# Kernel tuning notes

Measured on AMD Instinct MI355X. Metric: run time of the kernel, lower is better.

Reference implementation:

```python
import jax, jax.numpy as jnp
import numpy as np

N = 20000       # num_nodes
E = 200000      # ~ N*N*0.0005 directed edges from erdos_renyi
IN = 64         # in_channels
HID = 128       # hidden_channels (per head)
H = 4           # heads
OUT = 10        # out_channels
K1 = 10000      # ceil(0.5*N) nodes kept by pool1 (single graph -> static)
K2 = 5000       # ceil(0.5*K1) kept by pool2
NEG_SLOPE = 0.2 # PyG GATConv default negative_slope


def setup_inputs() -> dict:
    key = jax.random.key(0)
    ks = jax.random.split(key, 16)
    def glorot(k, shp, fan):
        return (jax.random.normal(k, shp, jnp.float32) / np.sqrt(fan)).astype(jnp.float32)
    x = jax.random.normal(ks[0], (N, IN), jnp.float32)
    edge_index = jax.random.randint(ks[1], (2, E), 0, N, dtype=jnp.int32)
    batch = jnp.zeros((N,), jnp.int32)
    W1 = glorot(ks[2], (IN, H * HID), IN)
    a_src1 = glorot(ks[3], (H, HID), HID)
    a_dst1 = glorot(ks[4], (H, HID), HID)
    b1 = jnp.zeros((H * HID,), jnp.float32)
    pw1 = glorot(ks[5], (H * HID,), H * HID)
    W2 = glorot(ks[6], (H * HID, H * HID), H * HID)
    a_src2 = glorot(ks[7], (H, HID), HID)
    a_dst2 = glorot(ks[8], (H, HID), HID)
    b2 = jnp.zeros((H * HID,), jnp.float32)
    pw2 = glorot(ks[9], (H * HID,), H * HID)
    Wl = glorot(ks[10], (H * HID, OUT), H * HID)
    bl = jnp.zeros((OUT,), jnp.float32)
    return dict(x=x, edge_index=edge_index, batch=batch,
                W1=W1, a_src1=a_src1, a_dst1=a_dst1, b1=b1, pw1=pw1,
                W2=W2, a_src2=a_src2, a_dst2=a_dst2, b2=b2, pw2=pw2,
                Wl=Wl, bl=bl)


def _gat(x, src, dst, emask, W, a_src, a_dst, bias):
    """PyG GATConv: gather -> LeakyReLU edge score -> scatter-softmax over dst -> scatter-add.
    Self-loops added (PyG default). emask marks valid edges (invalid edges point at node 0)."""
    n = x.shape[0]
    Hh, C = a_src.shape
    h = (x @ W).reshape(n, Hh, C)                      # [n,H,C]
    asrc = jnp.einsum('nhc,hc->nh', h, a_src)          # [n,H]
    adst = jnp.einsum('nhc,hc->nh', h, a_dst)
    loops = jnp.arange(n, dtype=src.dtype)
    sa = jnp.concatenate([src, loops])                 # [E+n]
    da = jnp.concatenate([dst, loops])
    ma = jnp.concatenate([emask, jnp.ones((n,), bool)])
    logit = jax.nn.leaky_relu(asrc[sa] + adst[da], negative_slope=NEG_SLOPE)  # [E+n,H]
    logit = jnp.where(ma[:, None], logit, -1e9)
    mx = jax.ops.segment_max(logit, da, num_segments=n)        # every node has a self-loop
    e = jnp.where(ma[:, None], jnp.exp(logit - mx[da]), 0.0)
    den = jax.ops.segment_sum(e, da, num_segments=n)
    alpha = e / den[da]                                         # [E+n,H]
    msg = (alpha[:, :, None] * h[sa]).reshape(-1, Hh * C)       # [E+n,H*C]
    return jax.ops.segment_sum(msg, da, num_segments=n) + bias  # concat heads + bias


def _topk_pool(x, src, dst, emask, w, k):
    """PyG TopKPooling (single graph): score = tanh(x.w/||w||), keep top-k nodes,
    scale kept features by score, relabel & mask edges between kept nodes."""
    score = jnp.tanh((x @ w) / jnp.linalg.norm(w))     # [n]
    vals, perm = jax.lax.top_k(score, k)
    xn = x[perm] * vals[:, None]                       # [k,F]
    remap = jnp.full((x.shape[0],), -1, jnp.int32).at[perm].set(jnp.arange(k, dtype=jnp.int32))
    s2 = remap[src]
    d2 = remap[dst]
    m2 = emask & (s2 >= 0) & (d2 >= 0)
    return xn, jnp.where(m2, s2, 0), jnp.where(m2, d2, 0), m2


def reference(x, edge_index, batch, W1, a_src1, a_dst1, b1, pw1,
              W2, a_src2, a_dst2, b2, pw2, Wl, bl):
    src = edge_index[0]
    dst = edge_index[1]
    mask = jnp.ones((src.shape[0],), bool)
    h = jax.nn.elu(_gat(x, src, dst, mask, W1, a_src1, a_dst1, b1))
    h, src, dst, mask = _topk_pool(h, src, dst, mask, pw1, K1)
    h = jax.nn.elu(_gat(h, src, dst, mask, W2, a_src2, a_dst2, b2))
    h, src, dst, mask = _topk_pool(h, src, dst, mask, pw2, K2)
    g = jnp.mean(h, axis=0, keepdims=True)             # global_mean_pool, single graph
    return g @ Wl + bl                                  # [1, OUT]
```

## Files before the change

### kernel.cpp

```cpp
#include <hip/hip_runtime.h>
#include <math.h>

#define N_NODES 20000
#define E_EDGES 200000
#define K1_KEEP 10000
#define K2_KEEP 5000
#define HIDC 128
#define NHEAD 4
#define FDIM 512
#define NEG 0.2f
#define BSTRIDE 64
#define SELCAP 20
#define MPAD 10112
#define FR_GRID 250
#define FR_RPB 40

typedef _Float16 half8 __attribute__((ext_vector_type(8)));
typedef _Float16 half4 __attribute__((ext_vector_type(4)));
typedef float f32x4 __attribute__((ext_vector_type(4)));

__device__ __forceinline__ float leaky(float x){ return x > 0.f ? x : NEG * x; }
__device__ __forceinline__ float elu(float x){ return x > 0.f ? x : expm1f(x); }
__device__ __forceinline__ unsigned ordkey(float f){
    unsigned u = __float_as_uint(f);
    return (u & 0x80000000u) ? ~u : (u | 0x80000000u);
}

template<int K, int COLB, int AMODE, bool GATHER, bool CLEAR>
__global__ __launch_bounds__(256) void gemm_tile(const float* __restrict__ A,
        const float* __restrict__ W, _Float16* __restrict__ out,
        const int* __restrict__ gidx, const float* __restrict__ gsc,
        const float* __restrict__ avS, const float* __restrict__ avD,
        float* __restrict__ asrc, float* __restrict__ adst, int n,
        int ngemm, int* __restrict__ ctmp, int cn,
        const float* __restrict__ cw, float* __restrict__ cinvn)
{
    int t = threadIdx.x;
    int bid = blockIdx.x;
    if constexpr (CLEAR){
        if (bid >= ngemm){
            __shared__ float redc[4];
            int b2 = bid - ngemm;
            int i = b2 * 256 + t;
            if (i < cn) ctmp[i] = 0;
            if (b2 == 0){
                float s = cw[t] * cw[t] + cw[t + 256] * cw[t + 256];
#pragma unroll
                for (int off = 32; off > 0; off >>= 1) s += __shfl_xor(s, off);
                if ((t & 63) == 0) redc[t >> 6] = s;
                __syncthreads();
                if (t == 0) *cinvn = rsqrtf(redc[0] + redc[1] + redc[2] + redc[3]);
            }
            return;
        }
    }
    constexpr int NR = COLB / 16;
    constexpr int WPT = COLB / 32;
    constexpr int BPR = 512 / COLB;
    __shared__ float At[32][68];
    __shared__ float Wt[32][COLB];
    int row0 = (bid / BPR) * 64;
    int col0 = (bid % BPR) * COLB;
    int tr = t >> 4;
    int tc = t & 15;
    float acc[4][NR] = {};

    int arow[2]; float asc[2];
#pragma unroll
    for (int i = 0; i < 2; ++i){
        int r = (t + i * 256) >> 3;
        int gr = row0 + r;
        arow[i] = -1; asc[i] = 1.f;
        if (gr < n){
            if (GATHER){ arow[i] = gidx[gr]; asc[i] = gsc[arow[i]]; }
            else arow[i] = gr;
        }
    }

    float4 pa[2], pw[WPT];
#pragma unroll
    for (int i = 0; i < 2; ++i){
        int kq = (t + i * 256) & 7;
        pa[i] = make_float4(0.f, 0.f, 0.f, 0.f);
        if (arow[i] >= 0){
            pa[i] = *reinterpret_cast<const float4*>(&A[(size_t)arow[i] * K + kq * 4]);
            if (GATHER){ pa[i].x *= asc[i]; pa[i].y *= asc[i]; pa[i].z *= asc[i]; pa[i].w *= asc[i]; }
        }
    }
#pragma unroll
    for (int i = 0; i < WPT; ++i){
        int s = t + i * 256; int k = s / (COLB / 4), c4 = s % (COLB / 4);
        pw[i] = *reinterpret_cast<const float4*>(&W[(size_t)k * 512 + col0 + c4 * 4]);
    }

    for (int kc = 0; kc < K; kc += 32){
#pragma unroll
        for (int i = 0; i < 2; ++i){
            int s = t + i * 256; int r = s >> 3, kq = s & 7;
            At[kq * 4 + 0][r] = pa[i].x;
            At[kq * 4 + 1][r] = pa[i].y;
            At[kq * 4 + 2][r] = pa[i].z;
            At[kq * 4 + 3][r] = pa[i].w;
        }
#pragma unroll
        for (int i = 0; i < WPT; ++i){
            int s = t + i * 256; int k = s / (COLB / 4), c4 = s % (COLB / 4);
            *reinterpret_cast<float4*>(&Wt[k][c4 * 4]) = pw[i];
        }
        __syncthreads();
        if (kc + 32 < K){
            int kn = kc + 32;
#pragma unroll
            for (int i = 0; i < 2; ++i){
                int kq = (t + i * 256) & 7;
                pa[i] = make_float4(0.f, 0.f, 0.f, 0.f);
                if (arow[i] >= 0){
                    pa[i] = *reinterpret_cast<const float4*>(&A[(size_t)arow[i] * K + kn + kq * 4]);
                    if (GATHER){ pa[i].x *= asc[i]; pa[i].y *= asc[i]; pa[i].z *= asc[i]; pa[i].w *= asc[i]; }
                }
            }
#pragma unroll
            for (int i = 0; i < WPT; ++i){
                int s = t + i * 256; int k = s / (COLB / 4), c4 = s % (COLB / 4);
                pw[i] = *reinterpret_cast<const float4*>(&W[(size_t)(kn + k) * 512 + col0 + c4 * 4]);
            }
        }
#pragma unroll 8
        for (int kk = 0; kk < 32; ++kk){
            float4 a = *reinterpret_cast<const float4*>(&At[kk][tr * 4]);
            float af[4] = {a.x, a.y, a.z, a.w};
            float wf[NR];
            {
                float4 w0 = *reinterpret_cast<const float4*>(&Wt[kk][tc * 4]);
                wf[0] = w0.x; wf[1] = w0.y; wf[2] = w0.z; wf[3] = w0.w;
                if constexpr (NR == 8){
                    float4 w1 = *reinterpret_cast<const float4*>(&Wt[kk][tc * 4 + 64]);
                    wf[4] = w1.x; wf[5] = w1.y; wf[6] = w1.z; wf[7] = w1.w;
                }
            }
#pragma unroll
            for (int r = 0; r < 4; ++r)
#pragma unroll
                for (int c = 0; c < NR; ++c) acc[r][c] += af[r] * wf[c];
        }
        __syncthreads();
    }
#pragma unroll
    for (int r = 0; r < 4; ++r){
        int gr = row0 + 4 * tr + r;
        if (gr < n){
            half4 h0, h1q;
#pragma unroll
            for (int c = 0; c < 4; ++c) h0[c] = (_Float16)acc[r][c];
            *reinterpret_cast<half4*>(&out[(size_t)gr * 512 + col0 + tc * 4]) = h0;
            if constexpr (NR == 8){
#pragma unroll
                for (int c = 0; c < 4; ++c) h1q[c] = (_Float16)acc[r][4 + c];
                *reinterpret_cast<half4*>(&out[(size_t)gr * 512 + col0 + 64 + tc * 4]) = h1q;
            }
        }
    }
    if constexpr (AMODE == 1){
        int head = col0 >> 7;
        const float* as = avS + head * HIDC;
        const float* ad = avD + head * HIDC;
#pragma unroll
        for (int r = 0; r < 4; ++r){
            float s = 0.f, d = 0.f;
#pragma unroll
            for (int c = 0; c < 4; ++c){
                s += acc[r][c] * as[4 * tc + c];
                d += acc[r][c] * ad[4 * tc + c];
                s += acc[r][4 + c] * as[64 + 4 * tc + c];
                d += acc[r][4 + c] * ad[64 + 4 * tc + c];
            }
#pragma unroll
            for (int off = 1; off < 16; off <<= 1){ s += __shfl_xor(s, off); d += __shfl_xor(d, off); }
            int gr = row0 + 4 * tr + r;
            if (tc == 0 && gr < n){ asrc[gr * 4 + head] = s; adst[gr * 4 + head] = d; }
        }
    }
}

__global__ __launch_bounds__(256) void prep_w2(const float* __restrict__ W2,
        _Float16* __restrict__ B0, _Float16* __restrict__ B1)
{
    __shared__ float tile[32][33];
    int bn = blockIdx.x & 15, bk = blockIdx.x >> 4;
    int n0 = bn * 32, k0 = bk * 32;
    int t = threadIdx.x;
    int j = t & 31, i0 = t >> 5;
#pragma unroll
    for (int ii = 0; ii < 32; ii += 8)
        tile[i0 + ii][j] = W2[(size_t)(k0 + i0 + ii) * 512 + n0 + j];
    __syncthreads();
#pragma unroll
    for (int ii = 0; ii < 32; ii += 8){
        float v = tile[j][i0 + ii];
        _Float16 h0 = (_Float16)v;
        _Float16 h1 = (_Float16)(v - (float)h0);
        size_t o = (size_t)(n0 + i0 + ii) * 512 + k0 + j;
        B0[o] = h0; B1[o] = h1;
    }
}

__global__ __launch_bounds__(256) void prep_a(const float* __restrict__ out1,
        const int* __restrict__ oldi, const float* __restrict__ score,
        _Float16* __restrict__ A0, _Float16* __restrict__ A1)
{
    int tid = blockIdx.x * 256 + threadIdx.x;
    int r = tid >> 6, kq = (tid & 63) << 3;
    half8 v0 = (half8)0, v1 = (half8)0;
    if (r < K1_KEEP){
        int o = oldi[r];
        float sc = score[o];
        const float4* p = reinterpret_cast<const float4*>(&out1[(size_t)o * 512 + kq]);
        float4 x0 = p[0], x1 = p[1];
        float vals[8] = {x0.x, x0.y, x0.z, x0.w, x1.x, x1.y, x1.z, x1.w};
#pragma unroll
        for (int j = 0; j < 8; ++j){
            float v = vals[j] * sc;
            _Float16 h = (_Float16)v;
            v0[j] = h;
            v1[j] = (_Float16)(v - (float)h);
        }
    }
    *reinterpret_cast<half8*>(&A0[(size_t)r * 512 + kq]) = v0;
    *reinterpret_cast<half8*>(&A1[(size_t)r * 512 + kq]) = v1;
}

__global__ __launch_bounds__(256, 2) void gemm2_mfma(
        const _Float16* __restrict__ A0, const _Float16* __restrict__ A1,
        const _Float16* __restrict__ B0, const _Float16* __restrict__ B1,
        const float* __restrict__ avS, const float* __restrict__ avD,
        _Float16* __restrict__ C, float* __restrict__ asrc, float* __restrict__ adst)
{
    __shared__ _Float16 smem[2][4][128][32];
    int t = threadIdx.x;
    int l = t & 63, w = t >> 6;
    int wr = w >> 1, wc = w & 1;
    int bidn = blockIdx.x & 3, bidm = blockIdx.x >> 2;
    int row0 = bidm * 128, col0 = bidn * 128;

    const _Float16* plane = (w == 0) ? A0 : (w == 1) ? A1 : (w == 2) ? B0 : B1;
    int prow0 = (w < 2) ? row0 : col0;
    int mloc = l >> 2;
    int gsw = (l & 3) ^ (mloc & 3);
    const _Float16* gbase = plane + (size_t)(prow0 + mloc) * 512 + gsw * 8;

    f32x4 acc[4][4];
#pragma unroll
    for (int m = 0; m < 4; ++m)
#pragma unroll
        for (int n = 0; n < 4; ++n) acc[m][n] = (f32x4){0.f, 0.f, 0.f, 0.f};

    auto stage = [&](int buf, int chunk){
        const _Float16* src = gbase + chunk * 32;
        char* db = (char*)&smem[buf][w][0][0];
#pragma unroll
        for (int i = 0; i < 8; ++i)
            __builtin_amdgcn_global_load_lds(
                (const __attribute__((address_space(1))) void*)(src + (size_t)i * 8192),
                (__attribute__((address_space(3))) void*)(db + i * 1024), 16, 0, 0);
    };

    int rb = (l & 15) * 64 + (((l >> 4) ^ (l & 3)) * 16);
    const char* sb = (const char*)smem;

    stage(0, 0);
    __syncthreads();
    for (int c = 0; c < 16; ++c){
        int buf = c & 1;
        if (c < 15) stage(buf ^ 1, c + 1);
        const char* base = sb + buf * 32768;
        half8 a0[4], a1[4], b0[4], b1[4];
#pragma unroll
        for (int m = 0; m < 4; ++m){
            a0[m] = *(const half8*)(base +         wr * 4096 + m * 1024 + rb);
            a1[m] = *(const half8*)(base +  8192 + wr * 4096 + m * 1024 + rb);
            b0[m] = *(const half8*)(base + 16384 + wc * 4096 + m * 1024 + rb);
            b1[m] = *(const half8*)(base + 24576 + wc * 4096 + m * 1024 + rb);
        }
#pragma unroll
        for (int m = 0; m < 4; ++m)
#pragma unroll
            for (int n = 0; n < 4; ++n)
                acc[m][n] = __builtin_amdgcn_mfma_f32_16x16x32_f16(a0[m], b0[n], acc[m][n], 0, 0, 0);
#pragma unroll
        for (int m = 0; m < 4; ++m)
#pragma unroll
            for (int n = 0; n < 4; ++n)
                acc[m][n] = __builtin_amdgcn_mfma_f32_16x16x32_f16(a0[m], b1[n], acc[m][n], 0, 0, 0);
#pragma unroll
        for (int m = 0; m < 4; ++m)
#pragma unroll
            for (int n = 0; n < 4; ++n)
                acc[m][n] = __builtin_amdgcn_mfma_f32_16x16x32_f16(a1[m], b0[n], acc[m][n], 0, 0, 0);
        __syncthreads();
    }

    int head = bidn;
    const float* asv = avS + head * HIDC + wc * 64;
    const float* adv = avD + head * HIDC + wc * 64;
    int lc = l & 15, lg = l >> 4;
    int rbase = row0 + wr * 64;
    int cbase = col0 + wc * 64;
#pragma unroll
    for (int m = 0; m < 4; ++m){
#pragma unroll
        for (int q = 0; q < 4; ++q){
            int row = rbase + m * 16 + lg * 4 + q;
            bool ok = row < K1_KEEP;
            float s = 0.f, d = 0.f;
#pragma unroll
            for (int n = 0; n < 4; ++n){
                float v = acc[m][n][q];
                int cc = n * 16 + lc;
                if (ok) C[(size_t)row * 512 + cbase + cc] = (_Float16)v;
                s += v * asv[cc];
                d += v * adv[cc];
            }
#pragma unroll
            for (int off = 1; off < 16; off <<= 1){
                s += __shfl_xor(s, off);
                d += __shfl_xor(d, off);
            }
            if (ok && lc == 0){
                asrc[row * 8 + head * 2 + wc] = s;
                adst[row * 8 + head * 2 + wc] = d;
            }
        }
    }
}

__global__ void edge_fill(const int* __restrict__ src, const int* __restrict__ dst, int e,
                          int* __restrict__ tmp, int* __restrict__ csr){
    int i = blockIdx.x * 256 + threadIdx.x;
    if (i >= e) return;
    int d = dst[i];
    int pos = atomicAdd(&tmp[d], 1);
    if (pos < BSTRIDE) csr[d * BSTRIDE + pos] = src[i];
}

template<bool FILTER>
__global__ __launch_bounds__(256) void gat_fused(const _Float16* __restrict__ h,
        const float* __restrict__ asrc, const float* __restrict__ adst,
        const int* __restrict__ degs, const int* __restrict__ csr,
        const int* __restrict__ oldi, const int* __restrict__ remap,
        const float* __restrict__ bias, const float* __restrict__ pw,
        const float* __restrict__ invn, float* __restrict__ out,
        float* __restrict__ score, int n)
{
    int node = blockIdx.x * 4 + (threadIdx.x >> 6);
    int lane = threadIdx.x & 63;
    if (node >= n) return;
    int od = FILTER ? oldi[node] : node;
    int deg = degs[od]; if (deg > BSTRIDE) deg = BSTRIDE;
    int e0 = od * BSTRIDE;
    int ph = lane & 3;
    int pe = lane >> 2;
    float adn, sown;
    if (FILTER){
        float2 dv = *reinterpret_cast<const float2*>(&adst[(size_t)node * 8 + ph * 2]);
        float2 sv = *reinterpret_cast<const float2*>(&asrc[(size_t)node * 8 + ph * 2]);
        adn = dv.x + dv.y; sown = sv.x + sv.y;
    } else {
        adn = adst[node * 4 + ph]; sown = asrc[node * 4 + ph];
    }
    float slog = leaky(sown + adn);
    int sreg[4];
    float mx = slog;
#pragma unroll
    for (int blk = 0; blk < 4; ++blk){
        int j = blk * 16 + pe;
        int s = -1;
        if (j < deg){
            s = csr[e0 + j];
            if (FILTER) s = remap[s];
            if (s >= 0){
                float av;
                if (FILTER){
                    float2 v = *reinterpret_cast<const float2*>(&asrc[(size_t)s * 8 + ph * 2]);
                    av = v.x + v.y;
                } else av = asrc[s * 4 + ph];
                mx = fmaxf(mx, leaky(av + adn));
            }
        }
        sreg[blk] = s;
    }
#pragma unroll
    for (int off = 4; off < 64; off <<= 1) mx = fmaxf(mx, __shfl_xor(mx, off));
    float aexp[4];
    float lsum = 0.f;
#pragma unroll
    for (int blk = 0; blk < 4; ++blk){
        float ex = 0.f;
        int s = sreg[blk];
        if (s >= 0){
            float av;
            if (FILTER){
                float2 v = *reinterpret_cast<const float2*>(&asrc[(size_t)s * 8 + ph * 2]);
                av = v.x + v.y;
            } else av = asrc[s * 4 + ph];
            ex = expf(leaky(av + adn) - mx);
        }
        aexp[blk] = ex;
        lsum += ex;
    }
#pragma unroll
    for (int off = 4; off < 64; off <<= 1) lsum += __shfl_xor(lsum, off);
    float es  = expf(slog - mx);
    float inv = 1.f / (lsum + es);

    int f0 = lane * 8;
    int hf = lane >> 4;
    float invh  = __shfl(inv, hf);
    float aself = __shfl(es, hf) * invh;
    float4 acc0, acc1;
    {
        half8 v = *reinterpret_cast<const half8*>(&h[(size_t)node * FDIM + f0]);
        acc0 = make_float4(aself * (float)v[0], aself * (float)v[1],
                           aself * (float)v[2], aself * (float)v[3]);
        acc1 = make_float4(aself * (float)v[4], aself * (float)v[5],
                           aself * (float)v[6], aself * (float)v[7]);
    }
#pragma unroll
    for (int blk = 0; blk < 4; ++blk){
        int base = blk * 16;
        if (base >= deg) break;
        int cnt = deg - base; if (cnt > 16) cnt = 16;
        for (int e = 0; e < cnt; ++e){
            int s = __shfl(sreg[blk], e * 4);
            if (FILTER && s < 0) continue;
            float al = __shfl(aexp[blk], e * 4 + hf) * invh;
            half8 u = *reinterpret_cast<const half8*>(&h[(size_t)s * FDIM + f0]);
            acc0.x += al * (float)u[0]; acc0.y += al * (float)u[1];
            acc0.z += al * (float)u[2]; acc0.w += al * (float)u[3];
            acc1.x += al * (float)u[4]; acc1.y += al * (float)u[5];
            acc1.z += al * (float)u[6]; acc1.w += al * (float)u[7];
        }
    }
    const float4* bp = reinterpret_cast<const float4*>(&bias[f0]);
    float4 b0 = bp[0], b1 = bp[1];
    float4 o0 = make_float4(elu(acc0.x + b0.x), elu(acc0.y + b0.y),
                            elu(acc0.z + b0.z), elu(acc0.w + b0.w));
    float4 o1 = make_float4(elu(acc1.x + b1.x), elu(acc1.y + b1.y),
                            elu(acc1.z + b1.z), elu(acc1.w + b1.w));
    float4* op = reinterpret_cast<float4*>(&out[(size_t)node * FDIM + f0]);
    op[0] = o0; op[1] = o1;
    const float4* wp = reinterpret_cast<const float4*>(&pw[f0]);
    float4 w0 = wp[0], w1 = wp[1];
    float s = o0.x * w0.x + o0.y * w0.y + o0.z * w0.z + o0.w * w0.w
            + o1.x * w1.x + o1.y * w1.y + o1.z * w1.z + o1.w * w1.w;
#pragma unroll
    for (int off = 32; off > 0; off >>= 1) s += __shfl_xor(s, off);
    if (lane == 0) score[node] = tanhf(s * (*invn));
}

__global__ __launch_bounds__(1024) void select_compact(const float* __restrict__ score,
        int n, int k, int* __restrict__ remap, int* __restrict__ oldidx,
        float* __restrict__ zbuf, int zn,
        const float* __restrict__ w, float* __restrict__ invn)
{
    __shared__ unsigned hist[16][256];
    __shared__ unsigned wtot[4];
    __shared__ unsigned s_prefix, s_rem, l_tie, l_keep;
    __shared__ float red2[16];
    int t = threadIdx.x;
    int wv = t >> 6;
    unsigned keys[SELCAP];
#pragma unroll
    for (int j = 0; j < SELCAP; ++j){
        int i = t + j * 1024;
        keys[j] = (i < n) ? ordkey(score[i]) : 0u;
    }
    if (t == 0){ s_prefix = 0u; s_rem = (unsigned)k; l_tie = 0u; l_keep = 0u; }
    for (int i = t; i < 16 * 256; i += 1024) ((unsigned*)hist)[i] = 0u;
    if (zbuf && t < zn) zbuf[t] = 0.f;
    __syncthreads();
    for (int pass = 3; pass >= 0; --pass){
        unsigned shift = (unsigned)pass * 8u;
        unsigned pmask = (pass == 3) ? 0u : (0xFFFFFFFFu << (shift + 8u));
        unsigned pref = s_prefix;
        unsigned remv = s_rem;
#pragma unroll
        for (int j = 0; j < SELCAP; ++j){
            int i = t + j * 1024;
            if (i < n && (keys[j] & pmask) == pref)
                atomicAdd(&hist[wv][(keys[j] >> shift) & 255u], 1u);
        }
        __syncthreads();
        unsigned c = 0, v = 0;
        if (t < 256){
            unsigned a = 0;
#pragma unroll
            for (int wq = 0; wq < 16; ++wq) a += hist[wq][t];
            c = a; v = a;
#pragma unroll
            for (int off = 1; off < 64; off <<= 1){
                unsigned o = __shfl_down(v, off);
                if ((t & 63) + off < 64) v += o;
            }
            if ((t & 63) == 0) wtot[t >> 6] = v;
        }
        __syncthreads();
        if (t < 256){
#pragma unroll
            for (int q = 0; q < 4; ++q)
                if (q > (t >> 6)) v += wtot[q];
            unsigned nxt = v - c;
            if (v >= remv && nxt < remv){
                s_prefix = pref | ((unsigned)t << shift);
                s_rem = remv - nxt;
            }
        }
        __syncthreads();
        if (pass > 0){
            for (int i = t; i < 16 * 256; i += 1024) ((unsigned*)hist)[i] = 0u;
            __syncthreads();
        }
    }
    unsigned T = s_prefix, ties = s_rem;
#pragma unroll
    for (int j = 0; j < SELCAP; ++j){
        int i = t + j * 1024;
        if (i >= n) continue;
        unsigned key = keys[j];
        int keep = 0;
        if (key > T) keep = 1;
        else if (key == T){
            unsigned tk = atomicAdd(&l_tie, 1u);
            if (tk < ties) keep = 1;
        }
        if (keep){
            int pos = (int)atomicAdd(&l_keep, 1u);
            remap[i] = pos;
            oldidx[pos] = i;
        } else remap[i] = -1;
    }
    if (w){
        float s = (t < 512) ? w[t] * w[t] : 0.f;
#pragma unroll
        for (int off = 32; off > 0; off >>= 1) s += __shfl_xor(s, off);
        if ((t & 63) == 0) red2[wv] = s;
        __syncthreads();
        if (t == 0){
            float a = 0.f;
            for (int i = 0; i < 16; ++i) a += red2[i];
            *invn = rsqrtf(a);
        }
    }
}

__global__ __launch_bounds__(512) void final_reduce(const float* __restrict__ x,
        const int* __restrict__ remap, const float* __restrict__ score,
        float* __restrict__ acc, const float* __restrict__ Wl)
{
    __shared__ float gsh[512];
    int t = threadIdx.x;
    int r0 = blockIdx.x * FR_RPB;
    float a = 0.f;
#pragma unroll
    for (int i = 0; i < FR_RPB; i += 4){
        int rr = r0 + i;
        float s0 = (remap[rr + 0] >= 0) ? score[rr + 0] : 0.f;
        float s1 = (remap[rr + 1] >= 0) ? score[rr + 1] : 0.f;
        float s2 = (remap[rr + 2] >= 0) ? score[rr + 2] : 0.f;
        float s3 = (remap[rr + 3] >= 0) ? score[rr + 3] : 0.f;
        float v0 = x[(size_t)(rr + 0) * FDIM + t];
        float v1 = x[(size_t)(rr + 1) * FDIM + t];
        float v2 = x[(size_t)(rr + 2) * FDIM + t];
        float v3 = x[(size_t)(rr + 3) * FDIM + t];
        a += v0 * s0 + v1 * s1 + v2 * s2 + v3 * s3;
    }
    gsh[t] = a;
    __syncthreads();
    int wv = t >> 6, lane = t & 63;
#pragma unroll
    for (int rep = 0; rep < 2; ++rep){
        int w = wv + rep * 8;
        if (w >= 10) break;
        float s = 0.f;
#pragma unroll
        for (int f = 0; f < 8; ++f) s += gsh[lane + f * 64] * Wl[(lane + f * 64) * 10 + w];
#pragma unroll
        for (int off = 32; off > 0; off >>= 1) s += __shfl_xor(s, off);
        if (lane == 0) atomicAdd(&acc[w * 32], s);
    }
}

__global__ __launch_bounds__(64) void final_out(const float* __restrict__ acc,
        const float* __restrict__ bl, float* __restrict__ out)
{
    int t = threadIdx.x;
    if (t < 10) out[t] = acc[t * 32] * (1.0f / K2_KEEP) + bl[t];
}

extern "C" void kernel_launch(void* const* d_in, const int* in_sizes, int n_in,
                              void* d_out, int out_size, void* d_ws, size_t ws_size,
                              hipStream_t stream)
{
    (void)in_sizes; (void)n_in; (void)out_size; (void)ws_size;
    const float* x   = (const float*)d_in[0];
    const int*   ei  = (const int*)  d_in[1];
    const float* W1  = (const float*)d_in[3];
    const float* as1 = (const float*)d_in[4];
    const float* ad1 = (const float*)d_in[5];
    const float* b1  = (const float*)d_in[6];
    const float* pw1 = (const float*)d_in[7];
    const float* W2  = (const float*)d_in[8];
    const float* as2 = (const float*)d_in[9];
    const float* ad2 = (const float*)d_in[10];
    const float* b2  = (const float*)d_in[11];
    const float* pw2 = (const float*)d_in[12];
    const float* Wl  = (const float*)d_in[13];
    const float* bl  = (const float*)d_in[14];
    const int* src1 = ei;
    const int* dst1 = ei + E_EDGES;

    char* wsb = (char*)d_ws;
    size_t off = 0;
    auto alloc = [&](size_t bytes) -> char* {
        char* p = wsb + off;
        off += (bytes + 255) & ~(size_t)255;
        return p;
    };
    _Float16* h1f = (_Float16*)alloc((size_t)N_NODES * FDIM * 2);
    float* out1 = (float*)alloc((size_t)N_NODES * FDIM * 4);
    float* asrc = (float*)alloc((size_t)N_NODES * NHEAD * 4);
    float* adst = (float*)alloc((size_t)N_NODES * NHEAD * 4);
    float* score= (float*)alloc((size_t)N_NODES * 4);
    float* invn = (float*)alloc(4);
    int* tmp  = (int*)alloc((size_t)N_NODES * 4);
    int* csr  = (int*)alloc((size_t)N_NODES * BSTRIDE * 4);
    int* remap= (int*)alloc((size_t)N_NODES * 4);
    int* oldi = (int*)alloc((size_t)K1_KEEP * 4);
    float* racc = (float*)alloc(320 * 4);
    _Float16* a0p = (_Float16*)alloc((size_t)MPAD * FDIM * 2);
    _Float16* a1p = (_Float16*)alloc((size_t)MPAD * FDIM * 2);
    _Float16* w2t0 = (_Float16*)alloc((size_t)FDIM * FDIM * 2);
    _Float16* w2t1 = (_Float16*)alloc((size_t)FDIM * FDIM * 2);
    _Float16* h2f = h1f;
    float* out2 = out1;

    int gx1 = (N_NODES + 63) / 64;
    int ngemm1 = gx1 * 4;
    int nclr = (N_NODES + 255) / 256;
    gemm_tile<64, 128, 1, false, true><<<ngemm1 + nclr, 256, 0, stream>>>(x, W1, h1f,
            nullptr, nullptr, as1, ad1, asrc, adst, N_NODES,
            ngemm1, tmp, N_NODES, pw1, invn);
    prep_w2<<<256, 256, 0, stream>>>(W2, w2t0, w2t1);
    edge_fill<<<(E_EDGES + 255) / 256, 256, 0, stream>>>(src1, dst1, E_EDGES, tmp, csr);
    gat_fused<false><<<(N_NODES + 3) / 4, 256, 0, stream>>>(h1f, asrc, adst, tmp, csr,
            nullptr, nullptr, b1, pw1, invn, out1, score, N_NODES);

    select_compact<<<1, 1024, 0, stream>>>(score, N_NODES, K1_KEEP, remap, oldi,
                                           nullptr, 0, pw2, invn);

    prep_a<<<MPAD / 4, 256, 0, stream>>>(out1, oldi, score, a0p, a1p);
    gemm2_mfma<<<(MPAD / 128) * 4, 256, 0, stream>>>(a0p, a1p, w2t0, w2t1,
            as2, ad2, h2f, asrc, adst);
    gat_fused<true><<<(K1_KEEP + 3) / 4, 256, 0, stream>>>(h2f, asrc, adst, tmp, csr,
            oldi, remap, b2, pw2, invn, out2, score, K1_KEEP);

    select_compact<<<1, 1024, 0, stream>>>(score, K1_KEEP, K2_KEEP, remap, oldi,
                                           racc, 320, nullptr, nullptr);
    final_reduce<<<FR_GRID, 512, 0, stream>>>(out2, remap, score, racc, Wl);
    final_out<<<1, 64, 0, stream>>>(racc, bl, (float*)d_out);
}
```

Measured before the change: 274.2 us.

## Move first GAT projection onto split-fp16 MFMA GEMM path

Replaces the fp32 SIMT tiled GEMM for x@W1 with the templated MFMA GEMM already used for layer two. Inputs and weights are split into hi/lo fp16 planes to keep accuracy close to fp32. The MFMA kernel writes attention logits in the 8-wide partial layout, so the unfiltered GAT path now reads that layout too. This adds two prep kernels (x split, W1 transpose/split merged with the counter clear and norm) and extra memory traffic in exchange for matrix-core throughput.

```diff
diff --git a/kernel.cpp b/kernel.cpp
--- a/kernel.cpp
+++ b/kernel.cpp
@@ -12,6 +12,7 @@
 #define BSTRIDE 64
 #define SELCAP 20
 #define MPAD 10112
+#define MPAD1 20096
 #define FR_GRID 250
 #define FR_RPB 40
 
@@ -26,159 +27,62 @@
     return (u & 0x80000000u) ? ~u : (u | 0x80000000u);
 }
 
-template<int K, int COLB, int AMODE, bool GATHER, bool CLEAR>
-__global__ __launch_bounds__(256) void gemm_tile(const float* __restrict__ A,
-        const float* __restrict__ W, _Float16* __restrict__ out,
-        const int* __restrict__ gidx, const float* __restrict__ gsc,
-        const float* __restrict__ avS, const float* __restrict__ avD,
-        float* __restrict__ asrc, float* __restrict__ adst, int n,
-        int ngemm, int* __restrict__ ctmp, int cn,
+__global__ __launch_bounds__(256) void prep_x(const float* __restrict__ x,
+        _Float16* __restrict__ X0, _Float16* __restrict__ X1)
+{
+    int tid = blockIdx.x * 256 + threadIdx.x;
+    int r = tid >> 3, c8 = (tid & 7) << 3;
+    half8 v0 = (half8)0, v1 = (half8)0;
+    if (r < N_NODES){
+        const float4* p = reinterpret_cast<const float4*>(&x[(size_t)r * 64 + c8]);
+        float4 x0 = p[0], x1 = p[1];
+        float vals[8] = {x0.x, x0.y, x0.z, x0.w, x1.x, x1.y, x1.z, x1.w};
+#pragma unroll
+        for (int j = 0; j < 8; ++j){
+            _Float16 h = (_Float16)vals[j];
+            v0[j] = h;
+            v1[j] = (_Float16)(vals[j] - (float)h);
+        }
+    }
+    *reinterpret_cast<half8*>(&X0[(size_t)r * 64 + c8]) = v0;
+    *reinterpret_cast<half8*>(&X1[(size_t)r * 64 + c8]) = v1;
+}
+
+__global__ __launch_bounds__(256) void prep_w1x(const float* __restrict__ W1,
+        _Float16* __restrict__ B0, _Float16* __restrict__ B1,
+        int* __restrict__ ctmp, int cn,
         const float* __restrict__ cw, float* __restrict__ cinvn)
 {
+    int bid = blockIdx.x;
     int t = threadIdx.x;
-    int bid = blockIdx.x;
-    if constexpr (CLEAR){
-        if (bid >= ngemm){
-            __shared__ float redc[4];
-            int b2 = bid - ngemm;
-            int i = b2 * 256 + t;
-            if (i < cn) ctmp[i] = 0;
-            if (b2 == 0){
-                float s = cw[t] * cw[t] + cw[t + 256] * cw[t + 256];
-#pragma unroll
-                for (int off = 32; off > 0; off >>= 1) s += __shfl_xor(s, off);
-                if ((t & 63) == 0) redc[t >> 6] = s;
-                __syncthreads();
-                if (t == 0) *cinvn = rsqrtf(redc[0] + redc[1] + redc[2] + redc[3]);
-            }
-            return;
-        }
-    }
-    constexpr int NR = COLB / 16;
-    constexpr int WPT = COLB / 32;
-    constexpr int BPR = 512 / COLB;
-    __shared__ float At[32][68];
-    __shared__ float Wt[32][COLB];
-    int row0 = (bid / BPR) * 64;
-    int col0 = (bid % BPR) * COLB;
-    int tr = t >> 4;
-    int tc = t & 15;
-    float acc[4][NR] = {};
-
-    int arow[2]; float asc[2];
-#pragma unroll
-    for (int i = 0; i < 2; ++i){
-        int r = (t + i * 256) >> 3;
-        int gr = row0 + r;
-        arow[i] = -1; asc[i] = 1.f;
-        if (gr < n){
-            if (GATHER){ arow[i] = gidx[gr]; asc[i] = gsc[arow[i]]; }
-            else arow[i] = gr;
-        }
-    }
-
-    float4 pa[2], pw[WPT];
-#pragma unroll
-    for (int i = 0; i < 2; ++i){
-        int kq = (t + i * 256) & 7;
-        pa[i] = make_float4(0.f, 0.f, 0.f, 0.f);
-        if (arow[i] >= 0){
-            pa[i] = *reinterpret_cast<const float4*>(&A[(size_t)arow[i] * K + kq * 4]);
-            if (GATHER){ pa[i].x *= asc[i]; pa[i].y *= asc[i]; pa[i].z *= asc[i]; pa[i].w *= asc[i]; }
-        }
-    }
-#pragma unroll
-    for (int i = 0; i < WPT; ++i){
-        int s = t + i * 256; int k = s / (COLB / 4), c4 = s % (COLB / 4);
-        pw[i] = *reinterpret_cast<const float4*>(&W[(size_t)k * 512 + col0 + c4 * 4]);
-    }
-
-    for (int kc = 0; kc < K; kc += 32){
-#pragma unroll
-        for (int i = 0; i < 2; ++i){
-            int s = t + i * 256; int r = s >> 3, kq = s & 7;
-            At[kq * 4 + 0][r] = pa[i].x;
-            At[kq * 4 + 1][r] = pa[i].y;
-            At[kq * 4 + 2][r] = pa[i].z;
-            At[kq * 4 + 3][r] = pa[i].w;
-        }
-#pragma unroll
-        for (int i = 0; i < WPT; ++i){
-            int s = t + i * 256; int k = s / (COLB / 4), c4 = s % (COLB / 4);
-            *reinterpret_cast<float4*>(&Wt[k][c4 * 4]) = pw[i];
-        }
-        __syncthreads();
-        if (kc + 32 < K){
-            int kn = kc + 32;
-#pragma unroll
-            for (int i = 0; i < 2; ++i){
-                int kq = (t + i * 256) & 7;
-                pa[i] = make_float4(0.f, 0.f, 0.f, 0.f);
-                if (arow[i] >= 0){
-                    pa[i] = *reinterpret_cast<const float4*>(&A[(size_t)arow[i] * K + kn + kq * 4]);
-                    if (GATHER){ pa[i].x *= asc[i]; pa[i].y *= asc[i]; pa[i].z *= asc[i]; pa[i].w *= asc[i]; }
-                }
-            }
-#pragma unroll
-            for (int i = 0; i < WPT; ++i){
-                int s = t + i * 256; int k = s / (COLB / 4), c4 = s % (COLB / 4);
-                pw[i] = *reinterpret_cast<const float4*>(&W[(size_t)(kn + k) * 512 + col0 + c4 * 4]);
-            }
-        }
-#pragma unroll 8
-        for (int kk = 0; kk < 32; ++kk){
-            float4 a = *reinterpret_cast<const float4*>(&At[kk][tr * 4]);
-            float af[4] = {a.x, a.y, a.z, a.w};
-            float wf[NR];
-            {
-                float4 w0 = *reinterpret_cast<const float4*>(&Wt[kk][tc * 4]);
-                wf[0] = w0.x; wf[1] = w0.y; wf[2] = w0.z; wf[3] = w0.w;
-                if constexpr (NR == 8){
-                    float4 w1 = *reinterpret_cast<const float4*>(&Wt[kk][tc * 4 + 64]);
-                    wf[4] = w1.x; wf[5] = w1.y; wf[6] = w1.z; wf[7] = w1.w;
-                }
-            }
-#pragma unroll
-            for (int r = 0; r < 4; ++r)
-#pragma unroll
-                for (int c = 0; c < NR; ++c) acc[r][c] += af[r] * wf[c];
-        }
-        __syncthreads();
-    }
-#pragma unroll
-    for (int r = 0; r < 4; ++r){
-        int gr = row0 + 4 * tr + r;
-        if (gr < n){
-            half4 h0, h1q;
-#pragma unroll
-            for (int c = 0; c < 4; ++c) h0[c] = (_Float16)acc[r][c];
-            *reinterpret_cast<half4*>(&out[(size_t)gr * 512 + col0 + tc * 4]) = h0;
-            if constexpr (NR == 8){
-#pragma unroll
-                for (int c = 0; c < 4; ++c) h1q[c] = (_Float16)acc[r][4 + c];
-                *reinterpret_cast<half4*>(&out[(size_t)gr * 512 + col0 + 64 + tc * 4]) = h1q;
-            }
-        }
-    }
-    if constexpr (AMODE == 1){
-        int head = col0 >> 7;
-        const float* as = avS + head * HIDC;
-        const float* ad = avD + head * HIDC;
-#pragma unroll
-        for (int r = 0; r < 4; ++r){
-            float s = 0.f, d = 0.f;
-#pragma unroll
-            for (int c = 0; c < 4; ++c){
-                s += acc[r][c] * as[4 * tc + c];
-                d += acc[r][c] * ad[4 * tc + c];
-                s += acc[r][4 + c] * as[64 + 4 * tc + c];
-                d += acc[r][4 + c] * ad[64 + 4 * tc + c];
-            }
-#pragma unroll
-            for (int off = 1; off < 16; off <<= 1){ s += __shfl_xor(s, off); d += __shfl_xor(d, off); }
-            int gr = row0 + 4 * tr + r;
-            if (tc == 0 && gr < n){ asrc[gr * 4 + head] = s; adst[gr * 4 + head] = d; }
-        }
+    if (bid < 32){
+        __shared__ float tile[32][33];
+        int bn = bid & 15, bk = bid >> 4;
+        int n0 = bn * 32, k0 = bk * 32;
+        int j = t & 31, i0 = t >> 5;
+#pragma unroll
+        for (int ii = 0; ii < 32; ii += 8)
+            tile[i0 + ii][j] = W1[(size_t)(k0 + i0 + ii) * 512 + n0 + j];
+        __syncthreads();
+#pragma unroll
+        for (int ii = 0; ii < 32; ii += 8){
+            float v = tile[j][i0 + ii];
+            _Float16 h0 = (_Float16)v;
+            _Float16 h1 = (_Float16)(v - (float)h0);
+            size_t o = (size_t)(n0 + i0 + ii) * 64 + k0 + j;
+            B0[o] = h0; B1[o] = h1;
+        }
+    } else if (bid < 32 + 79){
+        int i = (bid - 32) * 256 + t;
+        if (i < cn) ctmp[i] = 0;
+    } else {
+        __shared__ float redc[4];
+        float s = cw[t] * cw[t] + cw[t + 256] * cw[t + 256];
+#pragma unroll
+        for (int off = 32; off > 0; off >>= 1) s += __shfl_xor(s, off);
+        if ((t & 63) == 0) redc[t >> 6] = s;
+        __syncthreads();
+        if (t == 0) *cinvn = rsqrtf(redc[0] + redc[1] + redc[2] + redc[3]);
     }
 }
 
@@ -229,11 +133,13 @@
     *reinterpret_cast<half8*>(&A1[(size_t)r * 512 + kq]) = v1;
 }
 
-__global__ __launch_bounds__(256, 2) void gemm2_mfma(
+template<int KK>
+__global__ __launch_bounds__(256, 2) void gemm_mfma(
         const _Float16* __restrict__ A0, const _Float16* __restrict__ A1,
         const _Float16* __restrict__ B0, const _Float16* __restrict__ B1,
         const float* __restrict__ avS, const float* __restrict__ avD,
-        _Float16* __restrict__ C, float* __restrict__ asrc, float* __restrict__ adst)
+        _Float16* __restrict__ C, float* __restrict__ asrc, float* __restrict__ adst,
+        int nrows)
 {
     __shared__ _Float16 smem[2][4][128][32];
     int t = threadIdx.x;
@@ -246,7 +152,7 @@
     int prow0 = (w < 2) ? row0 : col0;
     int mloc = l >> 2;
     int gsw = (l & 3) ^ (mloc & 3);
-    const _Float16* gbase = plane + (size_t)(prow0 + mloc) * 512 + gsw * 8;
+    const _Float16* gbase = plane + (size_t)(prow0 + mloc) * KK + gsw * 8;
 
     f32x4 acc[4][4];
 #pragma unroll
@@ -260,18 +166,19 @@
 #pragma unroll
         for (int i = 0; i < 8; ++i)
             __builtin_amdgcn_global_load_lds(
-                (const __attribute__((address_space(1))) void*)(src + (size_t)i * 8192),
+                (const __attribute__((address_space(1))) void*)(src + (size_t)i * (KK * 16)),
                 (__attribute__((address_space(3))) void*)(db + i * 1024), 16, 0, 0);
     };
 
     int rb = (l & 15) * 64 + (((l >> 4) ^ (l & 3)) * 16);
     const char* sb = (const char*)smem;
 
+    constexpr int NCH = KK / 32;
     stage(0, 0);
     __syncthreads();
-    for (int c = 0; c < 16; ++c){
+    for (int c = 0; c < NCH; ++c){
         int buf = c & 1;
-        if (c < 15) stage(buf ^ 1, c + 1);
+        if (c < NCH - 1) stage(buf ^ 1, c + 1);
         const char* base = sb + buf * 32768;
         half8 a0[4], a1[4], b0[4], b1[4];
 #pragma unroll
@@ -310,7 +217,7 @@
 #pragma unroll
         for (int q = 0; q < 4; ++q){
             int row = rbase + m * 16 + lg * 4 + q;
-            bool ok = row < K1_KEEP;
+            bool ok = row < nrows;
             float s = 0.f, d = 0.f;
 #pragma unroll
             for (int n = 0; n < 4; ++n){
@@ -360,12 +267,10 @@
     int ph = lane & 3;
     int pe = lane >> 2;
     float adn, sown;
-    if (FILTER){
+    {
         float2 dv = *reinterpret_cast<const float2*>(&adst[(size_t)node * 8 + ph * 2]);
         float2 sv = *reinterpret_cast<const float2*>(&asrc[(size_t)node * 8 + ph * 2]);
         adn = dv.x + dv.y; sown = sv.x + sv.y;
-    } else {
-        adn = adst[node * 4 + ph]; sown = asrc[node * 4 + ph];
     }
     float slog = leaky(sown + adn);
     int sreg[4];
@@ -378,12 +283,8 @@
             s = csr[e0 + j];
             if (FILTER) s = remap[s];
             if (s >= 0){
-                float av;
-                if (FILTER){
-                    float2 v = *reinterpret_cast<const float2*>(&asrc[(size_t)s * 8 + ph * 2]);
-                    av = v.x + v.y;
-                } else av = asrc[s * 4 + ph];
-                mx = fmaxf(mx, leaky(av + adn));
+                float2 v = *reinterpret_cast<const float2*>(&asrc[(size_t)s * 8 + ph * 2]);
+                mx = fmaxf(mx, leaky(v.x + v.y + adn));
             }
         }
         sreg[blk] = s;
@@ -397,12 +298,8 @@
         float ex = 0.f;
         int s = sreg[blk];
         if (s >= 0){
-            float av;
-            if (FILTER){
-                float2 v = *reinterpret_cast<const float2*>(&asrc[(size_t)s * 8 + ph * 2]);
-                av = v.x + v.y;
-            } else av = asrc[s * 4 + ph];
-            ex = expf(leaky(av + adn) - mx);
+            float2 v = *reinterpret_cast<const float2*>(&asrc[(size_t)s * 8 + ph * 2]);
+            ex = expf(leaky(v.x + v.y + adn) - mx);
         }
         aexp[blk] = ex;
         lsum += ex;
@@ -627,8 +524,8 @@
     };
     _Float16* h1f = (_Float16*)alloc((size_t)N_NODES * FDIM * 2);
     float* out1 = (float*)alloc((size_t)N_NODES * FDIM * 4);
-    float* asrc = (float*)alloc((size_t)N_NODES * NHEAD * 4);
-    float* adst = (float*)alloc((size_t)N_NODES * NHEAD * 4);
+    float* asrc = (float*)alloc((size_t)N_NODES * 8 * 4);
+    float* adst = (float*)alloc((size_t)N_NODES * 8 * 4);
     float* score= (float*)alloc((size_t)N_NODES * 4);
     float* invn = (float*)alloc(4);
     int* tmp  = (int*)alloc((size_t)N_NODES * 4);
@@ -640,15 +537,17 @@
     _Float16* a1p = (_Float16*)alloc((size_t)MPAD * FDIM * 2);
     _Float16* w2t0 = (_Float16*)alloc((size_t)FDIM * FDIM * 2);
     _Float16* w2t1 = (_Float16*)alloc((size_t)FDIM * FDIM * 2);
+    _Float16* x0p = (_Float16*)alloc((size_t)MPAD1 * 64 * 2);
+    _Float16* x1p = (_Float16*)alloc((size_t)MPAD1 * 64 * 2);
+    _Float16* w1t0 = (_Float16*)alloc((size_t)FDIM * 64 * 2);
+    _Float16* w1t1 = (_Float16*)alloc((size_t)FDIM * 64 * 2);
     _Float16* h2f = h1f;
     float* out2 = out1;
 
-    int gx1 = (N_NODES + 63) / 64;
-    int ngemm1 = gx1 * 4;
-    int nclr = (N_NODES + 255) / 256;
-    gemm_tile<64, 128, 1, false, true><<<ngemm1 + nclr, 256, 0, stream>>>(x, W1, h1f,
-            nullptr, nullptr, as1, ad1, asrc, adst, N_NODES,
-            ngemm1, tmp, N_NODES, pw1, invn);
+    prep_x<<<MPAD1 * 8 / 256, 256, 0, stream>>>(x, x0p, x1p);
+    prep_w1x<<<112, 256, 0, stream>>>(W1, w1t0, w1t1, tmp, N_NODES, pw1, invn);
+    gemm_mfma<64><<<(MPAD1 / 128) * 4, 256, 0, stream>>>(x0p, x1p, w1t0, w1t1,
+            as1, ad1, h1f, asrc, adst, N_NODES);
     prep_w2<<<256, 256, 0, stream>>>(W2, w2t0, w2t1);
     edge_fill<<<(E_EDGES + 255) / 256, 256, 0, stream>>>(src1, dst1, E_EDGES, tmp, csr);
     gat_fused<false><<<(N_NODES + 3) / 4, 256, 0, stream>>>(h1f, asrc, adst, tmp, csr,
@@ -658,8 +557,8 @@
                                            nullptr, 0, pw2, invn);
 
     prep_a<<<MPAD / 4, 256, 0, stream>>>(out1, oldi, score, a0p, a1p);
-    gemm2_mfma<<<(MPAD / 128) * 4, 256, 0, stream>>>(a0p, a1p, w2t0, w2t1,
-            as2, ad2, h2f, asrc, adst);
+    gemm_mfma<512><<<(MPAD / 128) * 4, 256, 0, stream>>>(a0p, a1p, w2t0, w2t1,
+            as2, ad2, h2f, asrc, adst, K1_KEEP);
     gat_fused<true><<<(K1_KEEP + 3) / 4, 256, 0, stream>>>(h2f, asrc, adst, tmp, csr,
             oldi, remap, b2, pw2, invn, out2, score, K1_KEEP);
 
```

After: 271.0 us. About the same (-1.2%).
